# Kernel tuning notes

Hardware: AMD Instinct MI355X
Metric: run time of the kernel (lower is better)

Reference implementation:

```python
import jax, jax.numpy as jnp
import numpy as np

B, T, D, NH = 4, 2048, 1024, 16
HD = D // NH


def setup_inputs() -> dict:
    key = jax.random.key(0)
    ks = jax.random.split(key, 6)
    scale = 0.02
    x = jax.random.normal(ks[0], (B, T, D), dtype=jnp.float32)
    Wr = jax.random.normal(ks[1], (D, D), dtype=jnp.float32) * scale
    Wk = jax.random.normal(ks[2], (D, D), dtype=jnp.float32) * scale
    Wv = jax.random.normal(ks[3], (D, D), dtype=jnp.float32) * scale
    Ww = jax.random.normal(ks[4], (D, D), dtype=jnp.float32) * scale
    Wo = jax.random.normal(ks[5], (D, D), dtype=jnp.float32) * scale
    return {"x": x, "Wr": Wr, "Wk": Wk, "Wv": Wv, "Ww": Ww, "Wo": Wo}


def _rwkv7_forward(x, Wr, Wk, Wv, Ww, Wo):
    b, t, d = x.shape
    nh, hd = NH, d // NH
    # projections (F.linear: x @ W.T), no bias
    r = jax.nn.sigmoid(x @ Wr.T).reshape(b, t, nh, hd)
    k = (x @ Wk.T).reshape(b, t, nh, hd)
    v = (x @ Wv.T).reshape(b, t, nh, hd)
    w = (jax.nn.sigmoid(x @ Ww.T) * 0.99).reshape(b, t, nh, hd)

    def step(state, inp):
        # state: [B, nh, hd_v, hd_k]
        w_t, k_t, v_t, r_t = inp  # each [B, nh, hd]
        state = state * w_t[..., :, None] + v_t[..., :, None] * k_t[..., None, :]
        out_t = r_t * state.sum(-1)  # [B, nh, hd]
        return state, out_t

    seq = (jnp.moveaxis(w, 1, 0), jnp.moveaxis(k, 1, 0),
           jnp.moveaxis(v, 1, 0), jnp.moveaxis(r, 1, 0))  # time-major
    state0 = jnp.zeros((b, nh, hd, hd), dtype=x.dtype)
    _, outs = jax.lax.scan(step, state0, seq)  # [T, B, nh, hd]
    out = jnp.moveaxis(outs, 0, 1).reshape(b, t, d)

    # RMSNorm with eps=None -> torch uses dtype eps
    eps = jnp.asarray(jnp.finfo(out.dtype).eps, out.dtype)
    out = out * jax.lax.rsqrt(jnp.mean(out * out, axis=-1, keepdims=True) + eps)
    return out @ Wo.T


def reference(x, Wr, Wk, Wv, Ww, Wo):
    return _rwkv7_forward(x, Wr, Wk, Wv, Ww, Wo)
```

## Files before the change

### kernel.cpp

```cpp
#include <hip/hip_runtime.h>
#include <hip/hip_bf16.h>
#include <stdint.h>


#define BB 4
#define TT 2048
#define DD 1024
#define NHH 16
#define HDD 64
#define CC 64
#define LL 32
#define NCH 4096
#define MT (BB * TT)
#define ROWP 136

using bf16 = __hip_bfloat16;
typedef __attribute__((ext_vector_type(8))) short bfrag8;
typedef __attribute__((ext_vector_type(8))) unsigned short us8;
typedef __attribute__((ext_vector_type(4))) float f32x4;

__device__ __forceinline__ void async_ld16(const bf16* g, bf16* l) {
  __builtin_amdgcn_global_load_lds(
      (const __attribute__((address_space(1))) uint32_t*)g,
      (__attribute__((address_space(3))) uint32_t*)l, 16, 0, 0);
}

__device__ __forceinline__ float sigm(float x) {
  return __builtin_amdgcn_rcpf(1.0f + __expf(-x));
}
__device__ __forceinline__ float bf2f(bf16 h) {
  unsigned short u = *reinterpret_cast<unsigned short*>(&h);
  return __uint_as_float((unsigned)u << 16);
}
__device__ __forceinline__ float us2f(unsigned short u) {
  return __uint_as_float((unsigned)u << 16);
}
__device__ __forceinline__ unsigned short f2bfbits(float f) {
  bf16 b = __float2bfloat16(f);
  return *reinterpret_cast<unsigned short*>(&b);
}

__global__ __launch_bounds__(256)
void convert_kernel(const float* __restrict__ x,
                    const float* __restrict__ Wr, const float* __restrict__ Wv,
                    const float* __restrict__ Ww, const float* __restrict__ Wo,
                    const float* __restrict__ Wk,
                    bf16* __restrict__ x_c, bf16* __restrict__ W_c,
                    bf16* __restrict__ wks_bf)
{
  if (blockIdx.x < 64) {
    const int gid = blockIdx.x * 256 + threadIdx.x;
    const int h = gid >> 10, c = gid & 1023;
    float s = 0.0f;
    for (int j = 0; j < 64; ++j)
      s += Wk[(long)((h << 6) + j) * 1024 + c];
    wks_bf[gid] = __float2bfloat16(s);
    return;
  }
  const long g0 = (long)(blockIdx.x - 64) * 1024 + threadIdx.x;
#pragma unroll
  for (int it = 0; it < 4; ++it) {
    const long g = g0 + it * 256;
    const float* src; bf16* dst; long off4;
    if (g < 2097152) { src = x; dst = x_c; off4 = g; }
    else {
      long gg = g - 2097152;
      int wsel = (int)(gg >> 18);
      off4 = gg & 262143;
      src = (wsel == 0) ? Wr : (wsel == 1) ? Wv : (wsel == 2) ? Ww : Wo;
      dst = W_c + (long)wsel * 1048576;
    }
    float4 f = reinterpret_cast<const float4*>(src)[off4];
    ushort4 pk;
    pk.x = f2bfbits(f.x); pk.y = f2bfbits(f.y);
    pk.z = f2bfbits(f.z); pk.w = f2bfbits(f.w);
    reinterpret_cast<ushort4*>(dst)[off4] = pk;
  }
}

__device__ __forceinline__ void gemm_mainloop(
    const bf16* __restrict__ A, const bf16* __restrict__ W,
    int blockM, int blockN, bf16* a_sh, bf16* b_sh, f32x4 acc[4][4])
{
  const int tid    = threadIdx.x;
  const int wave   = tid >> 6;
  const int lane   = tid & 63;
  const int lane15 = lane & 15;
  const int quad   = lane >> 4;
  const int waveM  = wave >> 1;
  const int waveN  = wave & 1;
  const int s_row  = (wave << 5) + (lane >> 3);
  const int s_col  = (((lane & 7) ^ ((lane >> 3) & 7)) << 3);

  const bf16* gA = A + ((long)(blockM * 128) + s_row) * 1024 + s_col;
  const bf16* gW = W + ((long)(blockN * 128) + s_row) * 1024 + s_col;
  bf16* la = a_sh + wave * 2048;
  bf16* lb = b_sh + wave * 2048;

  const int rsw = lane15 & 7;

  for (int k0 = 0; k0 < 1024; k0 += 64) {
#pragma unroll
    for (int it = 0; it < 4; ++it) {
      async_ld16(gA + k0 + it * 8 * 1024, la + it * 512);
      async_ld16(gW + k0 + it * 8 * 1024, lb + it * 512);
    }
    __syncthreads();
#pragma unroll
    for (int kh = 0; kh < 2; ++kh) {
      bfrag8 af[4], bfv[4];
      const int pc = ((kh * 4 + quad) ^ rsw) << 3;
#pragma unroll
      for (int mi = 0; mi < 4; ++mi)
        af[mi] = *reinterpret_cast<const bfrag8*>(a_sh + (waveM*64 + mi*16 + lane15)*64 + pc);
#pragma unroll
      for (int ni = 0; ni < 4; ++ni)
        bfv[ni] = *reinterpret_cast<const bfrag8*>(b_sh + (waveN*64 + ni*16 + lane15)*64 + pc);
#pragma unroll
      for (int mi = 0; mi < 4; ++mi)
#pragma unroll
        for (int ni = 0; ni < 4; ++ni)
          acc[mi][ni] = __builtin_amdgcn_mfma_f32_16x16x32_bf16(af[mi], bfv[ni], acc[mi][ni], 0, 0, 0);
    }
    __syncthreads();
  }
}

__global__ __launch_bounds__(256, 2)
void proj_kernel(const bf16* __restrict__ X, const bf16* __restrict__ W_c,
                 bf16* __restrict__ r_t, bf16* __restrict__ v_t,
                 bf16* __restrict__ w_t,
                 const bf16* __restrict__ wks_bf, float* __restrict__ ksum)
{
  __shared__ __align__(16) bf16 sh[128 * ROWP];
  const int tid = threadIdx.x;

  if (blockIdx.x < 128) {
    const int kb   = blockIdx.x;
    const int wave = tid >> 6, lane = tid & 63;
    const int m0   = (kb * 4 + wave) * 16;
    const int kc   = (lane >> 4) * 8;
    const bf16* xp = X + (long)(m0 + (lane & 15)) * DD + kc;
    const bf16* wp = wks_bf + (lane & 15) * DD + kc;
    f32x4 acc0 = {}, acc1 = {};
#pragma unroll 4
    for (int k0 = 0; k0 < 1024; k0 += 64) {
      bfrag8 a0 = *reinterpret_cast<const bfrag8*>(xp + k0);
      bfrag8 b0 = *reinterpret_cast<const bfrag8*>(wp + k0);
      bfrag8 a1 = *reinterpret_cast<const bfrag8*>(xp + k0 + 32);
      bfrag8 b1 = *reinterpret_cast<const bfrag8*>(wp + k0 + 32);
      acc0 = __builtin_amdgcn_mfma_f32_16x16x32_bf16(a0, b0, acc0, 0, 0, 0);
      acc1 = __builtin_amdgcn_mfma_f32_16x16x32_bf16(a1, b1, acc1, 0, 0, 0);
    }
    const int h = lane & 15;
#pragma unroll
    for (int r = 0; r < 4; ++r) {
      const int m = m0 + (lane >> 4) * 4 + r;
      const int b = m >> 11, t = m & (TT - 1);
      ksum[((long)(b * NHH + h)) * TT + t] = acc0[r] + acc1[r];
    }
    return;
  }

  const int f  = blockIdx.x - 128;
  const int u  = f & 7;
  const int q  = f >> 3;
  const int n  = q & 7;
  const int p  = q >> 3;
  const int mh = p & 7;
  const int mode = p >> 3;
  const int m  = u + (mh << 3);

  const bf16* W = W_c + (long)mode * 1048576;
  f32x4 acc[4][4] = {};
  gemm_mainloop(X, W, m, n, sh, sh + 8192, acc);

  const int wave = tid >> 6, lane = tid & 63;
  const int lane15 = lane & 15, quad = lane >> 4;
  const int waveM = wave >> 1, waveN = wave & 1;
  bf16* outp = (mode == 0) ? r_t : (mode == 1) ? v_t : w_t;

#pragma unroll
  for (int mi = 0; mi < 4; ++mi) {
    const int mm0 = waveM*64 + mi*16 + quad*4;
#pragma unroll
    for (int ni = 0; ni < 4; ++ni) {
      const int nn = waveN*64 + ni*16 + lane15;
      float v0 = acc[mi][ni][0], v1 = acc[mi][ni][1];
      float v2 = acc[mi][ni][2], v3 = acc[mi][ni][3];
      if (mode == 0) { v0 = sigm(v0); v1 = sigm(v1); v2 = sigm(v2); v3 = sigm(v3); }
      else if (mode == 2) {
        v0 = sigm(v0)*0.99f; v1 = sigm(v1)*0.99f;
        v2 = sigm(v2)*0.99f; v3 = sigm(v3)*0.99f;
      }
      ushort4 pk;
      pk.x = f2bfbits(v0); pk.y = f2bfbits(v1);
      pk.z = f2bfbits(v2); pk.w = f2bfbits(v3);
      *reinterpret_cast<ushort4*>(sh + nn*ROWP + mm0) = pk;
    }
  }
  __syncthreads();

  const int nn_base = n * 128;
  const int mm_base = m * 128;
#pragma unroll
  for (int pp = 0; pp < 8; ++pp) {
    const int nn_l = pp*16 + (tid >> 4);
    const int mm_l = (tid & 15) * 8;
    us8 v = *reinterpret_cast<const us8*>(sh + nn_l*ROWP + mm_l);
    *reinterpret_cast<us8*>(outp + (long)(nn_base + nn_l) * MT + (mm_base + mm_l)) = v;
  }
}

__global__ __launch_bounds__(256)
void scanA_kernel(const bf16* __restrict__ v_t, const bf16* __restrict__ w_t,
                  const float* __restrict__ ksum,
                  float* __restrict__ Pbuf, float* __restrict__ Abuf)
{
  __shared__ float ks_sh[128];
  const int bh = blockIdx.x;
  const int b = bh >> 4, h = bh & 15;
  const int tid = threadIdx.x;
  const int i = tid & 63;
  const int cg = tid >> 6;
  const int chunk = blockIdx.y * 4 + cg;
  if (tid < 128) ks_sh[tid] = ksum[(long)bh * TT + blockIdx.y * 128 + tid];
  __syncthreads();
  const int ch = h * HDD + i;
  const long tbase = (long)ch * MT + b * TT + chunk * LL;
  us8 wv[4], vv[4];
#pragma unroll
  for (int q = 0; q < 4; ++q) {
    wv[q] = *reinterpret_cast<const us8*>(w_t + tbase + q*8);
    vv[q] = *reinterpret_cast<const us8*>(v_t + tbase + q*8);
  }
  const float* ksp = ks_sh + cg * LL;
  float s = 0.0f, P = 1.0f;
#pragma unroll
  for (int j = 0; j < LL; ++j) {
    float wf = us2f((unsigned short)wv[j>>3][j&7]);
    float vf = us2f((unsigned short)vv[j>>3][j&7]);
    s = fmaf(wf, s, vf * ksp[j]);
    P *= wf;
  }
  const int chn = bh * 64 + i;
  Pbuf[chunk * NCH + chn] = P;
  Abuf[chunk * NCH + chn] = s;
}

__global__ __launch_bounds__(256)
void scanB_kernel(const float* __restrict__ Pbuf, float* __restrict__ Abuf,
                  float* __restrict__ rowssq)
{
  const int tid  = threadIdx.x;
  const int lane = tid & 63;
  const int wch  = blockIdx.x * 4 + (tid >> 6);
  const int idx  = lane * NCH + wch;
  float p = Pbuf[idx];
  float a = Abuf[idx];
#pragma unroll
  for (int d = 1; d < 64; d <<= 1) {
    float al = __shfl_up(a, d);
    float pl = __shfl_up(p, d);
    if (lane >= d) { a = fmaf(p, al, a); p *= pl; }
  }
  float carry = __shfl_up(a, 1);
  if (lane == 0) carry = 0.0f;
  Abuf[idx] = carry;
  if (blockIdx.x < 32) rowssq[blockIdx.x * 256 + tid] = 0.0f;
}

__global__ __launch_bounds__(256)
void scanC_kernel(const bf16* __restrict__ r_t, const bf16* __restrict__ v_t,
                  const bf16* __restrict__ w_t, const float* __restrict__ ksum,
                  const float* __restrict__ Abuf, bf16* __restrict__ so,
                  float* __restrict__ rowssq)
{
  __shared__ float ks_sh[128];
  const int bh = blockIdx.x;
  const int b = bh >> 4, h = bh & 15;
  const int tid = threadIdx.x;
  const int i = tid & 63;
  const int cg = tid >> 6;
  const int chunk = blockIdx.y * 4 + cg;
  if (tid < 128) ks_sh[tid] = ksum[(long)bh * TT + blockIdx.y * 128 + tid];
  __syncthreads();
  const int ch = h * HDD + i;
  const long tbase = (long)ch * MT + b * TT + chunk * LL;
  us8 wv[4], vv[4], rv[4];
#pragma unroll
  for (int q = 0; q < 4; ++q) {
    wv[q] = *reinterpret_cast<const us8*>(w_t + tbase + q*8);
    vv[q] = *reinterpret_cast<const us8*>(v_t + tbase + q*8);
    rv[q] = *reinterpret_cast<const us8*>(r_t + tbase + q*8);
  }
  const float* ksp = ks_sh + cg * LL;
  const int chn = bh * 64 + i;
  float s = Abuf[chunk * NCH + chn];
  const long obase = (long)(b * TT + chunk * LL) * DD + ch;
#pragma unroll
  for (int j = 0; j < LL; ++j) {
    float wf = us2f((unsigned short)wv[j>>3][j&7]);
    float vf = us2f((unsigned short)vv[j>>3][j&7]);
    float rf = us2f((unsigned short)rv[j>>3][j&7]);
    s = fmaf(wf, s, vf * ksp[j]);
    unsigned short ob = f2bfbits(rf * s);
    *reinterpret_cast<unsigned short*>(so + obase + (long)j * DD) = ob;
    float vfo = us2f(ob);
    float ss = vfo * vfo;
#pragma unroll
    for (int msk = 1; msk <= 32; msk <<= 1) ss += __shfl_xor(ss, msk);
    if (i == 0) atomicAdd(&rowssq[b * TT + chunk * LL + j], ss);
  }
}

__global__ __launch_bounds__(256, 2)
void out_gemm_kernel(const bf16* __restrict__ A, const bf16* __restrict__ Wo_c,
                     const float* __restrict__ rowssq, float* __restrict__ out)
{
  __shared__ __align__(16) bf16 a_sh[128*64];
  __shared__ __align__(16) bf16 b_sh[128*64];
  const int f  = blockIdx.x;
  const int u  = f & 7;
  const int q  = f >> 3;
  const int n  = q & 7;
  const int mh = q >> 3;
  const int m  = u + (mh << 3);

  f32x4 acc[4][4] = {};
  gemm_mainloop(A, Wo_c, m, n, a_sh, b_sh, acc);

  const int tid = threadIdx.x;
  const int wave = tid >> 6, lane = tid & 63;
  const int lane15 = lane & 15, quad = lane >> 4;
  const int waveM = wave >> 1, waveN = wave & 1;
  const int m_base = m * 128 + waveM * 64;
  const int n_base = n * 128 + waveN * 64;
#pragma unroll
  for (int mi = 0; mi < 4; ++mi)
#pragma unroll
    for (int r = 0; r < 4; ++r) {
      int mm = m_base + mi*16 + quad*4 + r;
      float sc = rsqrtf(rowssq[mm] * (1.0f / DD) + 1.1920929e-07f);
#pragma unroll
      for (int ni = 0; ni < 4; ++ni) {
        int nn = n_base + ni*16 + lane15;
        out[(long)mm * DD + nn] = acc[mi][ni][r] * sc;
      }
    }
}

extern "C" void kernel_launch(void* const* d_in, const int* in_sizes, int n_in,
                              void* d_out, int out_size, void* d_ws, size_t ws_size,
                              hipStream_t stream) {
  const float* x  = (const float*)d_in[0];
  const float* Wr = (const float*)d_in[1];
  const float* Wk = (const float*)d_in[2];
  const float* Wv = (const float*)d_in[3];
  const float* Ww = (const float*)d_in[4];
  const float* Wo = (const float*)d_in[5];

  const long NELT = (long)BB * TT * DD;
  bf16*  x_c  = (bf16*)d_ws;
  bf16*  W_c  = x_c + NELT;
  bf16*  v_t  = W_c + 4 * 1048576;
  float* ksum = (float*)(v_t + NELT);
  bf16*  wks_bf = (bf16*)(ksum + (long)BB * NHH * TT);
  float* Pbuf = (float*)(wks_bf + NHH * DD) + 8192;
  float* Abuf = Pbuf + (long)CC * NCH;
  float* rowssq = (float*)W_c;

  bf16*  r_t  = (bf16*)d_out;
  bf16*  w_t  = (bf16*)d_out + NELT;
  bf16*  so   = x_c;
  float* out  = (float*)d_out;

  convert_kernel<<<dim3(3136), 256, 0, stream>>>(x, Wr, Wv, Ww, Wo, Wk, x_c, W_c, wks_bf);
  proj_kernel<<<dim3(1664), 256, 0, stream>>>(x_c, W_c, r_t, v_t, w_t, wks_bf, ksum);
  scanA_kernel<<<dim3(64, 16), 256, 0, stream>>>(v_t, w_t, ksum, Pbuf, Abuf);
  scanB_kernel<<<dim3(1024), 256, 0, stream>>>(Pbuf, Abuf, rowssq);
  scanC_kernel<<<dim3(64, 16), 256, 0, stream>>>(r_t, v_t, w_t, ksum, Abuf, so, rowssq);
  out_gemm_kernel<<<dim3(512), 256, 0, stream>>>(so, W_c + 3 * 1048576, rowssq, out);
}
```

Measured before the change: 218.3 us.

## Fuse chunk carry scan into scanC, removing the scanB kernel launch

```diff
diff --git a/kernel.cpp b/kernel.cpp
--- a/kernel.cpp
+++ b/kernel.cpp
@@ -215,7 +215,8 @@
 __global__ __launch_bounds__(256)
 void scanA_kernel(const bf16* __restrict__ v_t, const bf16* __restrict__ w_t,
                   const float* __restrict__ ksum,
-                  float* __restrict__ Pbuf, float* __restrict__ Abuf)
+                  float* __restrict__ Pbuf, float* __restrict__ Abuf,
+                  float* __restrict__ rowssq)
 {
   __shared__ float ks_sh[128];
   const int bh = blockIdx.x;
@@ -225,6 +226,7 @@
   const int cg = tid >> 6;
   const int chunk = blockIdx.y * 4 + cg;
   if (tid < 128) ks_sh[tid] = ksum[(long)bh * TT + blockIdx.y * 128 + tid];
+  if (blockIdx.y == 0 && tid < 128) rowssq[bh * 128 + tid] = 0.0f;
   __syncthreads();
   const int ch = h * HDD + i;
   const long tbase = (long)ch * MT + b * TT + chunk * LL;
@@ -249,42 +251,42 @@
 }
 
 __global__ __launch_bounds__(256)
-void scanB_kernel(const float* __restrict__ Pbuf, float* __restrict__ Abuf,
-                  float* __restrict__ rowssq)
-{
-  const int tid  = threadIdx.x;
-  const int lane = tid & 63;
-  const int wch  = blockIdx.x * 4 + (tid >> 6);
-  const int idx  = lane * NCH + wch;
-  float p = Pbuf[idx];
-  float a = Abuf[idx];
-#pragma unroll
-  for (int d = 1; d < 64; d <<= 1) {
-    float al = __shfl_up(a, d);
-    float pl = __shfl_up(p, d);
-    if (lane >= d) { a = fmaf(p, al, a); p *= pl; }
-  }
-  float carry = __shfl_up(a, 1);
-  if (lane == 0) carry = 0.0f;
-  Abuf[idx] = carry;
-  if (blockIdx.x < 32) rowssq[blockIdx.x * 256 + tid] = 0.0f;
-}
-
-__global__ __launch_bounds__(256)
 void scanC_kernel(const bf16* __restrict__ r_t, const bf16* __restrict__ v_t,
                   const bf16* __restrict__ w_t, const float* __restrict__ ksum,
-                  const float* __restrict__ Abuf, bf16* __restrict__ so,
-                  float* __restrict__ rowssq)
+                  const float* __restrict__ Pbuf, const float* __restrict__ Abuf,
+                  bf16* __restrict__ so, float* __restrict__ rowssq)
 {
   __shared__ float ks_sh[128];
+  __shared__ float carry_sh[64][5];
   const int bh = blockIdx.x;
   const int b = bh >> 4, h = bh & 15;
   const int tid = threadIdx.x;
   const int i = tid & 63;
   const int cg = tid >> 6;
-  const int chunk = blockIdx.y * 4 + cg;
-  if (tid < 128) ks_sh[tid] = ksum[(long)bh * TT + blockIdx.y * 128 + tid];
+  const int yb = blockIdx.y;
+  const int chunk = yb * 4 + cg;
+  if (tid < 128) ks_sh[tid] = ksum[(long)bh * TT + yb * 128 + tid];
+
+  {
+    const int w = tid >> 6, lane = tid & 63;
+    for (int chl = 0; chl < 16; ++chl) {
+      const int ch = w * 16 + chl;
+      const int idx = lane * NCH + bh * 64 + ch;
+      float p = Pbuf[idx];
+      float a = Abuf[idx];
+#pragma unroll
+      for (int d = 1; d < 64; d <<= 1) {
+        float al = __shfl_up(a, d);
+        float pl = __shfl_up(p, d);
+        if (lane >= d) { a = fmaf(p, al, a); p *= pl; }
+      }
+      float carry = __shfl_up(a, 1);
+      if (lane == 0) carry = 0.0f;
+      if ((lane >> 2) == yb) carry_sh[ch][lane & 3] = carry;
+    }
+  }
   __syncthreads();
+
   const int ch = h * HDD + i;
   const long tbase = (long)ch * MT + b * TT + chunk * LL;
   us8 wv[4], vv[4], rv[4];
@@ -295,8 +297,7 @@
     rv[q] = *reinterpret_cast<const us8*>(r_t + tbase + q*8);
   }
   const float* ksp = ks_sh + cg * LL;
-  const int chn = bh * 64 + i;
-  float s = Abuf[chunk * NCH + chn];
+  float s = carry_sh[i][cg];
   const long obase = (long)(b * TT + chunk * LL) * DD + ch;
 #pragma unroll
   for (int j = 0; j < LL; ++j) {
@@ -377,8 +378,7 @@
 
   convert_kernel<<<dim3(3136), 256, 0, stream>>>(x, Wr, Wv, Ww, Wo, Wk, x_c, W_c, wks_bf);
   proj_kernel<<<dim3(1664), 256, 0, stream>>>(x_c, W_c, r_t, v_t, w_t, wks_bf, ksum);
-  scanA_kernel<<<dim3(64, 16), 256, 0, stream>>>(v_t, w_t, ksum, Pbuf, Abuf);
-  scanB_kernel<<<dim3(1024), 256, 0, stream>>>(Pbuf, Abuf, rowssq);
-  scanC_kernel<<<dim3(64, 16), 256, 0, stream>>>(r_t, v_t, w_t, ksum, Abuf, so, rowssq);
+  scanA_kernel<<<dim3(64, 16), 256, 0, stream>>>(v_t, w_t, ksum, Pbuf, Abuf, rowssq);
+  scanC_kernel<<<dim3(64, 16), 256, 0, stream>>>(r_t, v_t, w_t, ksum, Pbuf, Abuf, so, rowssq);
   out_gemm_kernel<<<dim3(512), 256, 0, stream>>>(so, W_c + 3 * 1048576, rowssq, out);
 }
```

After: 223.5 us. 2.4% more time.
